# Optimization experiments

Measured on AMD Instinct MI355X. Metric: run time of the kernel, lower is better.

Reference implementation:

```python
import jax, jax.numpy as jnp
import numpy as np

# static multi-scale config (Deformable-DETR encoder, 1024x1024 image, strides 8/16/32/64)
SPATIAL_SHAPES = np.array([[128, 128], [64, 64], [32, 32], [16, 16]])  # (L, 2) = (h, w)
NUM_HEADS, NUM_LEVELS, NUM_POINTS = 8, 4, 4
EMBED, HEAD_DIM = 256, 32
NUM_KEYS = int(SPATIAL_SHAPES.prod(-1).sum())  # 21760


def _grid_sample(img, grid):
    """Bilinear grid_sample, padding_mode='zeros', align_corners=False.
    img: (BH, C, H, W); grid: (BH, Nq, P, 2) in [-1,1] -> (BH, C, Nq, P)."""
    BH, C, H, W = img.shape
    gx = (grid[..., 0] + 1.0) * (W / 2) - 0.5
    gy = (grid[..., 1] + 1.0) * (H / 2) - 0.5
    x0f, y0f = jnp.floor(gx), jnp.floor(gy)
    wx, wy = gx - x0f, gy - y0f
    x0, y0 = x0f.astype(jnp.int32), y0f.astype(jnp.int32)
    flat = img.reshape(BH, C, H * W)

    def gather(xi, yi, w):
        valid = (xi >= 0) & (xi < W) & (yi >= 0) & (yi < H)
        idx = jnp.clip(yi, 0, H - 1) * W + jnp.clip(xi, 0, W - 1)
        g = jnp.take_along_axis(flat, idx.reshape(BH, 1, -1), axis=2)
        g = g.reshape(BH, C, xi.shape[1], xi.shape[2])
        return g * (w * valid)[:, None]

    return (gather(x0, y0, (1 - wx) * (1 - wy)) + gather(x0 + 1, y0, wx * (1 - wy))
            + gather(x0, y0 + 1, (1 - wx) * wy) + gather(x0 + 1, y0 + 1, wx * wy))


def setup_inputs() -> dict:
    key = jax.random.key(0)
    ks = jax.random.split(key, 12)
    bs, nq = 1, NUM_KEYS
    s = 1.0 / np.sqrt(EMBED)
    return {
        "query": jax.random.normal(ks[0], (bs, nq, EMBED), jnp.float32),
        "query_pos": jax.random.normal(ks[1], (bs, nq, EMBED), jnp.float32),
        "value": jax.random.normal(ks[2], (bs, NUM_KEYS, EMBED), jnp.float32),
        "reference_points": jax.random.uniform(ks[3], (bs, nq, NUM_LEVELS, 2), jnp.float32),
        "spatial_shapes": jnp.asarray(SPATIAL_SHAPES, jnp.int32),
        "W_value": jax.random.normal(ks[4], (EMBED, EMBED), jnp.float32) * s,
        "b_value": jnp.zeros((EMBED,), jnp.float32),
        "W_off": jax.random.normal(ks[5], (NUM_HEADS * NUM_LEVELS * NUM_POINTS * 2, EMBED), jnp.float32) * 0.01,
        "b_off": jax.random.normal(ks[6], (NUM_HEADS * NUM_LEVELS * NUM_POINTS * 2,), jnp.float32),
        "W_attn": jax.random.normal(ks[7], (NUM_HEADS * NUM_LEVELS * NUM_POINTS, EMBED), jnp.float32) * s,
        "b_attn": jnp.zeros((NUM_HEADS * NUM_LEVELS * NUM_POINTS,), jnp.float32),
        "W_out": jax.random.normal(ks[8], (EMBED, EMBED), jnp.float32) * s,
        "b_out": jnp.zeros((EMBED,), jnp.float32),
    }


def reference(query, query_pos, value, reference_points, spatial_shapes,
              W_value, b_value, W_off, b_off, W_attn, b_attn, W_out, b_out):
    bs, nq, _ = query.shape
    identity = query
    q = query + query_pos  # pos_add
    v = value @ W_value.T + b_value  # value_proj: (bs, nk, E)
    v = v.reshape(bs, -1, NUM_HEADS, HEAD_DIM)

    offsets = (q @ W_off.T + b_off).reshape(bs, nq, NUM_HEADS, NUM_LEVELS, NUM_POINTS, 2)
    attn = (q @ W_attn.T + b_attn).reshape(bs, nq, NUM_HEADS, NUM_LEVELS * NUM_POINTS)
    attn = jax.nn.softmax(attn, axis=-1).reshape(bs, nq, NUM_HEADS, NUM_LEVELS, NUM_POINTS)

    # offset_normalizer = (w, h) per level; ref points are 2D -> loc = ref + off/norm
    normalizer = jnp.asarray(SPATIAL_SHAPES[:, ::-1].copy(), query.dtype)  # (L, 2)
    loc = reference_points[:, :, None, :, None, :] + offsets / normalizer[None, None, None, :, None, :]
    grids = 2.0 * loc - 1.0  # (bs, nq, H, L, P, 2)

    starts = np.concatenate([[0], np.cumsum(SPATIAL_SHAPES.prod(-1))])
    sampled = []
    for lvl in range(NUM_LEVELS):
        H_, W_ = int(SPATIAL_SHAPES[lvl, 0]), int(SPATIAL_SHAPES[lvl, 1])
        v_l = v[:, int(starts[lvl]):int(starts[lvl + 1])]  # (bs, H*W, heads, Dh)
        v_l = v_l.transpose(0, 2, 3, 1).reshape(bs * NUM_HEADS, HEAD_DIM, H_, W_)
        g_l = grids[:, :, :, lvl].transpose(0, 2, 1, 3, 4).reshape(bs * NUM_HEADS, nq, NUM_POINTS, 2)
        sampled.append(_grid_sample(v_l, g_l))  # (bs*H, Dh, nq, P)
    sampled = jnp.concatenate(sampled, axis=-1)  # (bs*H, Dh, nq, L*P)

    aw = attn.transpose(0, 2, 1, 3, 4).reshape(bs * NUM_HEADS, 1, nq, NUM_LEVELS * NUM_POINTS)
    out = (sampled * aw).sum(-1).reshape(bs, NUM_HEADS * HEAD_DIM, nq).transpose(0, 2, 1)
    out = out @ W_out.T + b_out  # output_proj
    return out + identity  # residual (dropout is identity at eval)
```

## Files before the change

kernel.cpp:

```cpp
#include <hip/hip_runtime.h>
#include <hip/hip_bf16.h>
#include <math.h>
#include <type_traits>

#define K_DIM 256
using bf16 = __hip_bfloat16;

typedef __attribute__((ext_vector_type(8))) short s8v;
typedef __attribute__((ext_vector_type(4))) float f4v;

__device__ __forceinline__ float b2f(unsigned short u) {
    return __uint_as_float(((unsigned)u) << 16);
}
__device__ __forceinline__ unsigned short f2b(float f) {
    unsigned u = __float_as_uint(f);
    unsigned r = 0x7FFFu + ((u >> 16) & 1u);
    return (unsigned short)((u + r) >> 16);
}
__device__ __forceinline__ float  ld1(const float* p) { return *p; }
__device__ __forceinline__ float  ld1(const bf16*  p) { return b2f(*(const unsigned short*)p); }
__device__ __forceinline__ float4 ld4(const float* p) { return *(const float4*)p; }
__device__ __forceinline__ float4 ld4(const bf16*  p) {
    ushort4 u = *(const ushort4*)p;
    return make_float4(b2f(u.x), b2f(u.y), b2f(u.z), b2f(u.w));
}
__device__ __forceinline__ s8v ldw8(const bf16* p) { return *(const s8v*)p; }

__device__ __forceinline__ bool detect_bf16(const unsigned* __restrict__ qw) {
    unsigned w = qw[threadIdx.x & 63];
    unsigned t = (w >> 8) & 0x7F;
    bool hit = (t >= 0x3Bu) && (t <= 0x42u);
    unsigned long long m = __ballot(hit);
    return __popcll(m) >= 32;
}

#define P1_TOTAL 164480
#define P_TOTAL  230272
__global__ __launch_bounds__(256) void k_prep(
    const unsigned* __restrict__ qd,
    const void* wv, const void* wo, const void* wa,
    const void* bv, const void* bo, const void* ba,
    const void* wout, const void* bout,
    bf16* __restrict__ dst1, bf16* __restrict__ dst2)
{
    const bool isb = detect_bf16(qd);
    const int i4 = (blockIdx.x * 256 + threadIdx.x) * 4;
    if (i4 >= P_TOTAL) return;
    const void* src; int off; bf16* dst;
    if (i4 < P1_TOTAL) {
        dst = dst1 + i4;
        if      (i4 < 65536)  { src = wv; off = i4; }
        else if (i4 < 131072) { src = wo; off = i4 - 65536; }
        else if (i4 < 163840) { src = wa; off = i4 - 131072; }
        else if (i4 < 164096) { src = bv; off = i4 - 163840; }
        else if (i4 < 164352) { src = bo; off = i4 - 164096; }
        else                  { src = ba; off = i4 - 164352; }
    } else {
        const int j = i4 - P1_TOTAL;
        dst = dst2 + j;
        if (j < 65536) { src = wout; off = j; }
        else           { src = bout; off = j - 65536; }
    }
    if (isb) {
        *(ushort4*)dst = *(const ushort4*)((const unsigned short*)src + off);
    } else {
        float4 v = *(const float4*)((const float*)src + off);
        *(ushort4*)dst = make_ushort4(f2b(v.x), f2b(v.y), f2b(v.z), f2b(v.w));
    }
}

template<typename AT, typename RT, typename CT, int NFRAG, bool ADD_A2, bool SPLIT,
         bool ADD_RES, bool HMAJOR, bool HM2, bool A1HM>
__device__ __forceinline__ void mfma_gemm_body(
    unsigned short* __restrict__ As, int bm,
    const AT* __restrict__ A1, const AT* __restrict__ A2,
    const bf16* __restrict__ W1, const bf16* __restrict__ bias1, CT* __restrict__ C1, int N1,
    const bf16* __restrict__ W2, const bf16* __restrict__ bias2, bf16* __restrict__ C2, int N2,
    const RT* __restrict__ Res, int Mtot)
{
    const int tid = threadIdx.x;

    {
        const AT* t1 = A1 + (size_t)bm * K_DIM;
        if constexpr (!ADD_A2 && std::is_same<AT, bf16>::value) {
            s8v r[4];
            #pragma unroll
            for (int j = 0; j < 4; ++j) {
                const int e = j * 2048 + tid * 8;
                const int row = e >> 8, col = e & 255;
                const bf16* src;
                if constexpr (A1HM)
                    src = (const bf16*)A1 +
                          ((size_t)(col >> 5) * (size_t)Mtot + (size_t)(bm + row)) * 32 + (col & 31);
                else
                    src = t1 + e;
                r[j] = *(const s8v*)src;
            }
            #pragma unroll
            for (int j = 0; j < 4; ++j) {
                const int e = j * 2048 + tid * 8;
                *(s8v*)&As[(e >> 8) * 264 + (e & 255)] = r[j];
            }
        } else {
            float4 ra[8], rb[8];
            #pragma unroll
            for (int j = 0; j < 8; ++j)
                ra[j] = ld4(t1 + j * 1024 + tid * 4);
            if (ADD_A2) {
                const AT* t2 = A2 + (size_t)bm * K_DIM;
                #pragma unroll
                for (int j = 0; j < 8; ++j)
                    rb[j] = ld4(t2 + j * 1024 + tid * 4);
            }
            #pragma unroll
            for (int j = 0; j < 8; ++j) {
                const int e = j * 1024 + tid * 4;
                float4 v = ra[j];
                if (ADD_A2) { v.x += rb[j].x; v.y += rb[j].y; v.z += rb[j].z; v.w += rb[j].w; }
                *(ushort4*)&As[(e >> 8) * 264 + (e & 255)] =
                    make_ushort4(f2b(v.x), f2b(v.y), f2b(v.z), f2b(v.w));
            }
        }
    }

    const int wv = tid >> 6;
    const int lane = tid & 63;
    const int n15 = lane & 15;
    const int quad = lane >> 4;

    const bf16* Wr[NFRAG];
    int col[NFRAG];
    #pragma unroll
    for (int f = 0; f < NFRAG; ++f) {
        const int c = (wv * NFRAG + f) * 16 + n15;
        col[f] = c;
        if (SPLIT && c >= N1) Wr[f] = W2 + (size_t)(c - N1) * K_DIM;
        else                  Wr[f] = W1 + (size_t)c * K_DIM;
    }

    s8v bcur[NFRAG], bnxt[NFRAG];
    #pragma unroll
    for (int f = 0; f < NFRAG; ++f) bcur[f] = ldw8(Wr[f] + quad * 8);

    float bv[NFRAG];
    #pragma unroll
    for (int f = 0; f < NFRAG; ++f) {
        const int c = col[f];
        const bool hi = SPLIT && (c >= N1);
        bv[f] = hi ? ld1(bias2 + (c - N1)) : ld1(bias1 + c);
    }

    float rres[NFRAG][8];
    if constexpr (ADD_RES) {
        #pragma unroll
        for (int f = 0; f < NFRAG; ++f)
            #pragma unroll
            for (int mi = 0; mi < 2; ++mi)
                #pragma unroll
                for (int r = 0; r < 4; ++r) {
                    const int m = bm + mi * 16 + quad * 4 + r;
                    rres[f][mi * 4 + r] = ld1(Res + (size_t)m * N1 + col[f]);
                }
    }

    __syncthreads();

    const f4v zz = {0.f, 0.f, 0.f, 0.f};
    f4v acc[2][NFRAG];
    #pragma unroll
    for (int mi = 0; mi < 2; ++mi)
        #pragma unroll
        for (int f = 0; f < NFRAG; ++f) acc[mi][f] = zz;

    #pragma unroll
    for (int kk = 0; kk < 8; ++kk) {
        const int k0 = kk * 32 + quad * 8;
        if (kk < 7) {
            #pragma unroll
            for (int f = 0; f < NFRAG; ++f) bnxt[f] = ldw8(Wr[f] + k0 + 32);
        }
        s8v a[2];
        #pragma unroll
        for (int mi = 0; mi < 2; ++mi)
            a[mi] = *(const s8v*)&As[(mi * 16 + n15) * 264 + k0];
        #pragma unroll
        for (int mi = 0; mi < 2; ++mi)
            #pragma unroll
            for (int f = 0; f < NFRAG; ++f)
                acc[mi][f] = __builtin_amdgcn_mfma_f32_16x16x32_bf16(a[mi], bcur[f], acc[mi][f], 0, 0, 0);
        if (kk < 7) {
            #pragma unroll
            for (int f = 0; f < NFRAG; ++f) bcur[f] = bnxt[f];
        }
    }

    __syncthreads();

    if constexpr (std::is_same<CT, float>::value) {
        float* Asf = (float*)As;
        #pragma unroll
        for (int pass = 0; pass < 2; ++pass) {
            #pragma unroll
            for (int f = 0; f < NFRAG; ++f)
                #pragma unroll
                for (int r = 0; r < 4; ++r) {
                    float v = acc[pass][f][r] + bv[f];
                    if (ADD_RES) v += rres[f][pass * 4 + r];
                    Asf[(quad * 4 + r) * 264 + col[f]] = v;
                }
            __syncthreads();
            {
                const int row = tid >> 4;
                const int c16 = tid & 15;
                float* dst = (float*)C1 + (size_t)(bm + pass * 16 + row) * 256;
                #pragma unroll
                for (int s = 0; s < 4; ++s) {
                    const int eo = (c16 + s * 16) * 4;
                    *(float4*)(dst + eo) = *(const float4*)(Asf + row * 264 + eo);
                }
            }
            __syncthreads();
        }
    } else {
        unsigned short* Asu = As;
        #pragma unroll
        for (int f = 0; f < NFRAG; ++f) {
            if (!SPLIT || col[f] < N1) {
                #pragma unroll
                for (int mi = 0; mi < 2; ++mi)
                    #pragma unroll
                    for (int r = 0; r < 4; ++r) {
                        float v = acc[mi][f][r] + bv[f];
                        if (ADD_RES) v += rres[f][mi * 4 + r];
                        Asu[(mi * 16 + quad * 4 + r) * 264 + col[f]] = f2b(v);
                    }
            }
        }
        __syncthreads();
        if constexpr (HMAJOR) {
            const int h = tid >> 5;
            const int t32 = tid & 31;
            bf16* dsth = C1 + ((size_t)h * Mtot + bm) * 32;
            #pragma unroll
            for (int s = 0; s < 4; ++s) {
                const int o16 = t32 + s * 32;
                const int row = o16 >> 2;
                const int ch8 = (o16 & 3) * 8;
                *(s8v*)(dsth + (size_t)row * 32 + ch8) =
                    *(const s8v*)(Asu + row * 264 + h * 32 + ch8);
            }
        } else {
            const int row = tid >> 3;
            const int c8 = tid & 7;
            bf16* dst = C1 + (size_t)(bm + row) * 256;
            #pragma unroll
            for (int s = 0; s < 4; ++s) {
                const int eo = (c8 + s * 8) * 8;
                *(s8v*)(dst + eo) = *(const s8v*)(Asu + row * 264 + eo);
            }
        }
        if constexpr (SPLIT) {
            __syncthreads();
            #pragma unroll
            for (int f = 0; f < NFRAG; ++f) {
                if (col[f] >= N1) {
                    #pragma unroll
                    for (int mi = 0; mi < 2; ++mi)
                        #pragma unroll
                        for (int r = 0; r < 4; ++r) {
                            float v = acc[mi][f][r] + bv[f];
                            Asu[(mi * 16 + quad * 4 + r) * 264 + (col[f] - N1)] = f2b(v);
                        }
                }
            }
            __syncthreads();
            const int h = tid >> 5;
            const int t32 = tid & 31;
            bf16* dsth = C2 + ((size_t)h * Mtot + bm) * 16;
            #pragma unroll
            for (int s = 0; s < 2; ++s) {
                const int o16 = t32 + s * 32;
                const int row = o16 >> 1;
                const int ch8 = (o16 & 1) * 8;
                *(s8v*)(dsth + (size_t)row * 16 + ch8) =
                    *(const s8v*)(Asu + row * 264 + h * 16 + ch8);
            }
        }
    }
}

__global__ __launch_bounds__(256) void k_gemm12(
    const unsigned* __restrict__ qd,
    const void* value, const void* query, const void* query_pos,
    const bf16* c_wv, const bf16* c_bv, bf16* vproj,
    const bf16* c_wo, const bf16* c_bo, bf16* osb,
    const bf16* c_wa, const bf16* c_ba, bf16* logit,
    int nb1, int Mtot)
{
    __shared__ __align__(16) unsigned short As[32 * 264];
    const bool isb = detect_bf16(qd);
    if ((int)blockIdx.x < nb1) {
        const int bm = blockIdx.x * 32;
        if (isb)
            mfma_gemm_body<bf16, float, bf16, 4, false, false, false, true, false, false>(As, bm,
                (const bf16*)value, nullptr, c_wv, c_bv, vproj, 256,
                nullptr, nullptr, nullptr, 0, nullptr, Mtot);
        else
            mfma_gemm_body<float, float, bf16, 4, false, false, false, true, false, false>(As, bm,
                (const float*)value, nullptr, c_wv, c_bv, vproj, 256,
                nullptr, nullptr, nullptr, 0, nullptr, Mtot);
    } else {
        const int bm = (blockIdx.x - nb1) * 32;
        if (isb)
            mfma_gemm_body<bf16, float, bf16, 6, true, true, false, true, true, false>(As, bm,
                (const bf16*)query, (const bf16*)query_pos, c_wo, c_bo, osb, 256,
                c_wa, c_ba, logit, 128, nullptr, Mtot);
        else
            mfma_gemm_body<float, float, bf16, 6, true, true, false, true, true, false>(As, bm,
                (const float*)query, (const float*)query_pos, c_wo, c_bo, osb, 256,
                c_wa, c_ba, logit, 128, nullptr, Mtot);
    }
}

__global__ __launch_bounds__(256) void k_gemm_final(
    const unsigned* __restrict__ qd, const bf16* A1,
    const bf16* W, const bf16* bias, const void* Res, void* C, int Mtot)
{
    __shared__ __align__(16) unsigned short As[32 * 264];
    const int bm = blockIdx.x * 32;
    if (detect_bf16(qd))
        mfma_gemm_body<bf16, bf16, bf16, 4, false, false, true, false, false, true>(As, bm,
            A1, nullptr, W, bias, (bf16*)C, 256,
            nullptr, nullptr, nullptr, 0, (const bf16*)Res, Mtot);
    else
        mfma_gemm_body<bf16, float, float, 4, false, false, true, false, false, true>(As, bm,
            A1, nullptr, W, bias, (float*)C, 256,
            nullptr, nullptr, nullptr, 0, (const float*)Res, Mtot);
}

struct SampLds {
    float    swgt[16][32][4];
    unsigned sidx[16][32][2];
};

__global__ __launch_bounds__(256) void k_sample(
    const unsigned* __restrict__ qd, const bf16* __restrict__ vproj,
    bf16* __restrict__ osb, const bf16* __restrict__ logits,
    const void* __restrict__ refp, int Mtot)
{
    __shared__ SampLds L;
    const bool isb = detect_bf16(qd);
    const int t  = threadIdx.x;
    const int p  = t >> 3;
    const int dg = t & 7;
    const int head = blockIdx.x & 7;
    const int qc   = blockIdx.x >> 3;
    const int q = qc * 32 + p;
    const size_t hm = (size_t)head * (size_t)Mtot;

    float f0, f1, f2, f3;
    {
        ushort4 u = *(const ushort4*)(osb + (hm + q) * 32 + dg * 4);
        f0 = b2f(u.x); f1 = b2f(u.y); f2 = b2f(u.z); f3 = b2f(u.w);
    }

    float p0, p1;
    {
        ushort2 lu = *(const ushort2*)(logits + (hm + q) * 16 + dg * 2);
        float l0 = b2f(lu.x), l1 = b2f(lu.y);
        float mx = fmaxf(l0, l1);
        mx = fmaxf(mx, __shfl_xor(mx, 1));
        mx = fmaxf(mx, __shfl_xor(mx, 2));
        mx = fmaxf(mx, __shfl_xor(mx, 4));
        float e0 = __expf(l0 - mx), e1 = __expf(l1 - mx);
        float s = e0 + e1;
        s += __shfl_xor(s, 1);
        s += __shfl_xor(s, 2);
        s += __shfl_xor(s, 4);
        const float inv = 1.f / s;
        p0 = e0 * inv; p1 = e1 * inv;
    }

    const int lv = dg >> 1;
    float rx, ry;
    if (isb) {
        rx = ld1((const bf16*)refp + (size_t)q * 8 + 2 * lv);
        ry = ld1((const bf16*)refp + (size_t)q * 8 + 2 * lv + 1);
    } else {
        rx = ld1((const float*)refp + (size_t)q * 8 + 2 * lv);
        ry = ld1((const float*)refp + (size_t)q * 8 + 2 * lv + 1);
    }

    #pragma unroll
    for (int tt = 0; tt < 2; ++tt) {
        const int i = dg * 2 + tt;
        const int l = i >> 2;
        const int WW = 128 >> l;
        const int st = (l == 0) ? 0 : (l == 1) ? 16384 : (l == 2) ? 20480 : 21504;
        const float ox = tt ? f2 : f0;
        const float oy = tt ? f3 : f1;
        const float aw = tt ? p1 : p0;
        const float gx = rx * (float)WW + ox - 0.5f;
        const float gy = ry * (float)WW + oy - 0.5f;
        const float x0f = floorf(gx);
        const float y0f = floorf(gy);
        const float wx = gx - x0f;
        const float wy = gy - y0f;
        const int x0 = (int)x0f;
        const int y0 = (int)y0f;
        const float ux0 = (x0 >= 0 && x0 < WW) ? (1.f - wx) : 0.f;
        const float ux1 = (x0 + 1 >= 0 && x0 + 1 < WW) ? wx : 0.f;
        const float uA = (x0 >= 0) ? ux0 : ux1;
        const float uB = (x0 >= 0) ? ux1 : 0.f;
        const int bx = min(max(x0, 0), WW - 1);
        const float vy0 = (y0 >= 0 && y0 < WW) ? 1.f : 0.f;
        const float vy1 = (y0 + 1 >= 0 && y0 + 1 < WW) ? 1.f : 0.f;
        const int yc0 = min(max(y0, 0), WW - 1);
        const int yc1 = min(max(y0 + 1, 0), WW - 1);
        const float cy0 = (1.f - wy) * vy0 * aw;
        const float cy1 = wy * vy1 * aw;
        *(float4*)L.swgt[i][p] = make_float4(uA * cy0, uB * cy0, uA * cy1, uB * cy1);
        *(uint2*)L.sidx[i][p] = make_uint2(
            (unsigned)(st + yc0 * WW + bx) * 64u,
            (unsigned)(st + yc1 * WW + bx) * 64u);
    }
    __syncthreads();

    const unsigned hb = (unsigned)(hm * 64) + (unsigned)dg * 16u;
    const char* vb = (const char*)vproj;

    uint2 iv[16];
    #pragma unroll
    for (int i = 0; i < 16; ++i) iv[i] = *(const uint2*)L.sidx[i][p];

    s8v r0[16], r1[16];
    #pragma unroll
    for (int i = 0; i < 16; ++i) {
        r0[i] = *(const s8v*)(vb + (size_t)(iv[i].x + hb));
        r1[i] = *(const s8v*)(vb + (size_t)(iv[i].y + hb));
    }

    const bool lo = (dg < 4);
    float acc[8] = {0.f, 0.f, 0.f, 0.f, 0.f, 0.f, 0.f, 0.f};
    #pragma unroll
    for (int i = 0; i < 16; ++i) {
        const float4 w = *(const float4*)L.swgt[i][p];
        const float w0 = lo ? w.x : w.y;
        const float w1 = lo ? w.z : w.w;
        #pragma unroll
        for (int k = 0; k < 8; ++k)
            acc[k] = fmaf(w0, b2f((unsigned short)r0[i][k]), acc[k]);
        #pragma unroll
        for (int k = 0; k < 8; ++k)
            acc[k] = fmaf(w1, b2f((unsigned short)r1[i][k]), acc[k]);
    }

    #pragma unroll
    for (int k = 0; k < 8; ++k) acc[k] += __shfl_xor(acc[k], 4);

    if (dg < 4) {
        s8v o;
        #pragma unroll
        for (int k = 0; k < 8; ++k) o[k] = (short)f2b(acc[k]);
        *(s8v*)(osb + (hm + q) * 32 + dg * 8) = o;
    }
}

extern "C" void kernel_launch(void* const* d_in, const int* in_sizes, int n_in,
                              void* d_out, int out_size, void* d_ws, size_t ws_size,
                              hipStream_t stream) {
    const void* query     = d_in[0];
    const void* query_pos = d_in[1];
    const void* value     = d_in[2];
    const void* refp      = d_in[3];
    const void* W_value = d_in[5];
    const void* b_value = d_in[6];
    const void* W_off   = d_in[7];
    const void* b_off   = d_in[8];
    const void* W_attn  = d_in[9];
    const void* b_attn  = d_in[10];
    const void* W_out   = d_in[11];
    const void* b_out   = d_in[12];
    const unsigned* qd = (const unsigned*)d_in[0];

    const int M = in_sizes[0] / 256;
    char* wsb = (char*)d_ws;

    bf16* vproj = (bf16*)wsb;
    bf16* osb   = (bf16*)(wsb + (size_t)M * 512);
    bf16* wc2   = (bf16*)(wsb + (size_t)M * 1024);
    bf16* logit = (bf16*)d_out;
    bf16* wc1   = (bf16*)((char*)d_out + (8u << 20));
    const bf16* c_wv = wc1;
    const bf16* c_wo = wc1 + 65536;
    const bf16* c_wa = wc1 + 131072;
    const bf16* c_bv = wc1 + 163840;
    const bf16* c_bo = wc1 + 164096;
    const bf16* c_ba = wc1 + 164352;

    dim3 blk(256, 1, 1);
    const int nb1 = M / 32;
    dim3 g12((unsigned)(2 * nb1), 1, 1);
    dim3 g32((unsigned)nb1, 1, 1);
    dim3 gs((unsigned)(M / 4), 1, 1);

    k_prep<<<dim3((P_TOTAL / 4 + 255) / 256), blk, 0, stream>>>(qd,
        W_value, W_off, W_attn, b_value, b_off, b_attn, W_out, b_out, wc1, wc2);
    k_gemm12<<<g12, blk, 0, stream>>>(qd, value, query, query_pos,
        c_wv, c_bv, vproj, c_wo, c_bo, osb, c_wa, c_ba, logit, nb1, M);
    k_sample<<<gs, blk, 0, stream>>>(qd, vproj, osb, logit, refp, M);
    k_gemm_final<<<g32, blk, 0, stream>>>(qd, osb, wc2, wc2 + 65536, query, d_out, M);
}
```

Baseline: 201.9 us.

## Double GEMM row tile to 64 and move residual add into coalesced epilogue

The GEMM body now processes 64 rows per block instead of 32, with four MFMA row fragments per wave, so each weight fragment loaded from global memory is reused across twice as many rows. This halves the block count and the total weight traffic. The residual is no longer gathered per element into registers before the main loop; it is read with vectorized, coalesced loads in a staged LDS epilogue and added there. The cost is more accumulator registers, a larger LDS tile and fewer blocks to spread across the GPU, which can lower occupancy.

```diff
diff --git a/kernel.cpp b/kernel.cpp
--- a/kernel.cpp
+++ b/kernel.cpp
@@ -83,9 +83,9 @@
     {
         const AT* t1 = A1 + (size_t)bm * K_DIM;
         if constexpr (!ADD_A2 && std::is_same<AT, bf16>::value) {
-            s8v r[4];
-            #pragma unroll
-            for (int j = 0; j < 4; ++j) {
+            s8v r[8];
+            #pragma unroll
+            for (int j = 0; j < 8; ++j) {
                 const int e = j * 2048 + tid * 8;
                 const int row = e >> 8, col = e & 255;
                 const bf16* src;
@@ -97,28 +97,31 @@
                 r[j] = *(const s8v*)src;
             }
             #pragma unroll
-            for (int j = 0; j < 4; ++j) {
+            for (int j = 0; j < 8; ++j) {
                 const int e = j * 2048 + tid * 8;
                 *(s8v*)&As[(e >> 8) * 264 + (e & 255)] = r[j];
             }
         } else {
-            float4 ra[8], rb[8];
-            #pragma unroll
-            for (int j = 0; j < 8; ++j)
-                ra[j] = ld4(t1 + j * 1024 + tid * 4);
-            if (ADD_A2) {
-                const AT* t2 = A2 + (size_t)bm * K_DIM;
+            const AT* t2 = ADD_A2 ? (A2 + (size_t)bm * K_DIM) : (const AT*)0;
+            #pragma unroll
+            for (int jb = 0; jb < 4; ++jb) {
+                float4 ra[4], rb[4];
                 #pragma unroll
-                for (int j = 0; j < 8; ++j)
-                    rb[j] = ld4(t2 + j * 1024 + tid * 4);
-            }
-            #pragma unroll
-            for (int j = 0; j < 8; ++j) {
-                const int e = j * 1024 + tid * 4;
-                float4 v = ra[j];
-                if (ADD_A2) { v.x += rb[j].x; v.y += rb[j].y; v.z += rb[j].z; v.w += rb[j].w; }
-                *(ushort4*)&As[(e >> 8) * 264 + (e & 255)] =
-                    make_ushort4(f2b(v.x), f2b(v.y), f2b(v.z), f2b(v.w));
+                for (int j = 0; j < 4; ++j)
+                    ra[j] = ld4(t1 + (jb * 4 + j) * 1024 + tid * 4);
+                if (ADD_A2) {
+                    #pragma unroll
+                    for (int j = 0; j < 4; ++j)
+                        rb[j] = ld4(t2 + (jb * 4 + j) * 1024 + tid * 4);
+                }
+                #pragma unroll
+                for (int j = 0; j < 4; ++j) {
+                    const int e = (jb * 4 + j) * 1024 + tid * 4;
+                    float4 v = ra[j];
+                    if (ADD_A2) { v.x += rb[j].x; v.y += rb[j].y; v.z += rb[j].z; v.w += rb[j].w; }
+                    *(ushort4*)&As[(e >> 8) * 264 + (e & 255)] =
+                        make_ushort4(f2b(v.x), f2b(v.y), f2b(v.z), f2b(v.w));
+                }
             }
         }
     }
@@ -150,25 +153,12 @@
         bv[f] = hi ? ld1(bias2 + (c - N1)) : ld1(bias1 + c);
     }
 
-    float rres[NFRAG][8];
-    if constexpr (ADD_RES) {
-        #pragma unroll
-        for (int f = 0; f < NFRAG; ++f)
-            #pragma unroll
-            for (int mi = 0; mi < 2; ++mi)
-                #pragma unroll
-                for (int r = 0; r < 4; ++r) {
-                    const int m = bm + mi * 16 + quad * 4 + r;
-                    rres[f][mi * 4 + r] = ld1(Res + (size_t)m * N1 + col[f]);
-                }
-    }
-
     __syncthreads();
 
     const f4v zz = {0.f, 0.f, 0.f, 0.f};
-    f4v acc[2][NFRAG];
-    #pragma unroll
-    for (int mi = 0; mi < 2; ++mi)
+    f4v acc[4][NFRAG];
+    #pragma unroll
+    for (int mi = 0; mi < 4; ++mi)
         #pragma unroll
         for (int f = 0; f < NFRAG; ++f) acc[mi][f] = zz;
 
@@ -179,12 +169,12 @@
             #pragma unroll
             for (int f = 0; f < NFRAG; ++f) bnxt[f] = ldw8(Wr[f] + k0 + 32);
         }
-        s8v a[2];
-        #pragma unroll
-        for (int mi = 0; mi < 2; ++mi)
+        s8v a[4];
+        #pragma unroll
+        for (int mi = 0; mi < 4; ++mi)
             a[mi] = *(const s8v*)&As[(mi * 16 + n15) * 264 + k0];
         #pragma unroll
-        for (int mi = 0; mi < 2; ++mi)
+        for (int mi = 0; mi < 4; ++mi)
             #pragma unroll
             for (int f = 0; f < NFRAG; ++f)
                 acc[mi][f] = __builtin_amdgcn_mfma_f32_16x16x32_bf16(a[mi], bcur[f], acc[mi][f], 0, 0, 0);
@@ -196,28 +186,35 @@
 
     __syncthreads();
 
-    if constexpr (std::is_same<CT, float>::value) {
+    if constexpr (ADD_RES) {
         float* Asf = (float*)As;
         #pragma unroll
-        for (int pass = 0; pass < 2; ++pass) {
+        for (int mi = 0; mi < 4; ++mi) {
             #pragma unroll
             for (int f = 0; f < NFRAG; ++f)
                 #pragma unroll
-                for (int r = 0; r < 4; ++r) {
-                    float v = acc[pass][f][r] + bv[f];
-                    if (ADD_RES) v += rres[f][pass * 4 + r];
-                    Asf[(quad * 4 + r) * 264 + col[f]] = v;
+                for (int r = 0; r < 4; ++r)
+                    Asf[(quad * 4 + r) * 264 + col[f]] = acc[mi][f][r] + bv[f];
+            __syncthreads();
+            #pragma unroll
+            for (int s = 0; s < 4; ++s) {
+                const int idx = s * 256 + tid;
+                const int row = idx >> 6;
+                const int c16 = idx & 63;
+                float4 o = *(const float4*)(Asf + row * 264 + c16 * 4);
+                const size_t m = (size_t)(bm + mi * 16 + row);
+                if constexpr (std::is_same<RT, bf16>::value) {
+                    ushort4 ru = *(const ushort4*)((const bf16*)Res + m * 256 + c16 * 4);
+                    o.x += b2f(ru.x); o.y += b2f(ru.y); o.z += b2f(ru.z); o.w += b2f(ru.w);
+                } else {
+                    float4 rf = *(const float4*)((const float*)Res + m * 256 + c16 * 4);
+                    o.x += rf.x; o.y += rf.y; o.z += rf.z; o.w += rf.w;
                 }
-            __syncthreads();
-            {
-                const int row = tid >> 4;
-                const int c16 = tid & 15;
-                float* dst = (float*)C1 + (size_t)(bm + pass * 16 + row) * 256;
-                #pragma unroll
-                for (int s = 0; s < 4; ++s) {
-                    const int eo = (c16 + s * 16) * 4;
-                    *(float4*)(dst + eo) = *(const float4*)(Asf + row * 264 + eo);
-                }
+                if constexpr (std::is_same<CT, float>::value)
+                    *(float4*)((float*)C1 + m * 256 + c16 * 4) = o;
+                else
+                    *(ushort4*)((bf16*)C1 + m * 256 + c16 * 4) =
+                        make_ushort4(f2b(o.x), f2b(o.y), f2b(o.z), f2b(o.w));
             }
             __syncthreads();
         }
@@ -227,13 +224,11 @@
         for (int f = 0; f < NFRAG; ++f) {
             if (!SPLIT || col[f] < N1) {
                 #pragma unroll
-                for (int mi = 0; mi < 2; ++mi)
+                for (int mi = 0; mi < 4; ++mi)
                     #pragma unroll
-                    for (int r = 0; r < 4; ++r) {
-                        float v = acc[mi][f][r] + bv[f];
-                        if (ADD_RES) v += rres[f][mi * 4 + r];
-                        Asu[(mi * 16 + quad * 4 + r) * 264 + col[f]] = f2b(v);
-                    }
+                    for (int r = 0; r < 4; ++r)
+                        Asu[(mi * 16 + quad * 4 + r) * 264 + col[f]] =
+                            f2b(acc[mi][f][r] + bv[f]);
             }
         }
         __syncthreads();
@@ -242,7 +237,7 @@
             const int t32 = tid & 31;
             bf16* dsth = C1 + ((size_t)h * Mtot + bm) * 32;
             #pragma unroll
-            for (int s = 0; s < 4; ++s) {
+            for (int s = 0; s < 8; ++s) {
                 const int o16 = t32 + s * 32;
                 const int row = o16 >> 2;
                 const int ch8 = (o16 & 3) * 8;
@@ -250,13 +245,13 @@
                     *(const s8v*)(Asu + row * 264 + h * 32 + ch8);
             }
         } else {
-            const int row = tid >> 3;
-            const int c8 = tid & 7;
-            bf16* dst = C1 + (size_t)(bm + row) * 256;
-            #pragma unroll
-            for (int s = 0; s < 4; ++s) {
-                const int eo = (c8 + s * 8) * 8;
-                *(s8v*)(dst + eo) = *(const s8v*)(Asu + row * 264 + eo);
+            #pragma unroll
+            for (int s = 0; s < 8; ++s) {
+                const int idx = s * 256 + tid;
+                const int row = idx >> 5;
+                const int c16 = idx & 31;
+                *(s8v*)(C1 + (size_t)(bm + row) * 256 + c16 * 8) =
+                    *(const s8v*)(Asu + row * 264 + c16 * 8);
             }
         }
         if constexpr (SPLIT) {
@@ -265,12 +260,11 @@
             for (int f = 0; f < NFRAG; ++f) {
                 if (col[f] >= N1) {
                     #pragma unroll
-                    for (int mi = 0; mi < 2; ++mi)
+                    for (int mi = 0; mi < 4; ++mi)
                         #pragma unroll
-                        for (int r = 0; r < 4; ++r) {
-                            float v = acc[mi][f][r] + bv[f];
-                            Asu[(mi * 16 + quad * 4 + r) * 264 + (col[f] - N1)] = f2b(v);
-                        }
+                        for (int r = 0; r < 4; ++r)
+                            Asu[(mi * 16 + quad * 4 + r) * 264 + (col[f] - N1)] =
+                                f2b(acc[mi][f][r] + bv[f]);
                 }
             }
             __syncthreads();
@@ -278,7 +272,7 @@
             const int t32 = tid & 31;
             bf16* dsth = C2 + ((size_t)h * Mtot + bm) * 16;
             #pragma unroll
-            for (int s = 0; s < 2; ++s) {
+            for (int s = 0; s < 4; ++s) {
                 const int o16 = t32 + s * 32;
                 const int row = o16 >> 1;
                 const int ch8 = (o16 & 1) * 8;
@@ -297,10 +291,10 @@
     const bf16* c_wa, const bf16* c_ba, bf16* logit,
     int nb1, int Mtot)
 {
-    __shared__ __align__(16) unsigned short As[32 * 264];
+    __shared__ __align__(16) unsigned short As[64 * 264];
     const bool isb = detect_bf16(qd);
     if ((int)blockIdx.x < nb1) {
-        const int bm = blockIdx.x * 32;
+        const int bm = blockIdx.x * 64;
         if (isb)
             mfma_gemm_body<bf16, float, bf16, 4, false, false, false, true, false, false>(As, bm,
                 (const bf16*)value, nullptr, c_wv, c_bv, vproj, 256,
@@ -310,7 +304,7 @@
                 (const float*)value, nullptr, c_wv, c_bv, vproj, 256,
                 nullptr, nullptr, nullptr, 0, nullptr, Mtot);
     } else {
-        const int bm = (blockIdx.x - nb1) * 32;
+        const int bm = (blockIdx.x - nb1) * 64;
         if (isb)
             mfma_gemm_body<bf16, float, bf16, 6, true, true, false, true, true, false>(As, bm,
                 (const bf16*)query, (const bf16*)query_pos, c_wo, c_bo, osb, 256,
@@ -326,8 +320,8 @@
     const unsigned* __restrict__ qd, const bf16* A1,
     const bf16* W, const bf16* bias, const void* Res, void* C, int Mtot)
 {
-    __shared__ __align__(16) unsigned short As[32 * 264];
-    const int bm = blockIdx.x * 32;
+    __shared__ __align__(16) unsigned short As[64 * 264];
+    const int bm = blockIdx.x * 64;
     if (detect_bf16(qd))
         mfma_gemm_body<bf16, bf16, bf16, 4, false, false, true, false, false, true>(As, bm,
             A1, nullptr, W, bias, (bf16*)C, 256,
@@ -499,9 +493,9 @@
     const bf16* c_ba = wc1 + 164352;
 
     dim3 blk(256, 1, 1);
-    const int nb1 = M / 32;
+    const int nb1 = M / 64;
     dim3 g12((unsigned)(2 * nb1), 1, 1);
-    dim3 g32((unsigned)nb1, 1, 1);
+    dim3 g64((unsigned)nb1, 1, 1);
     dim3 gs((unsigned)(M / 4), 1, 1);
 
     k_prep<<<dim3((P_TOTAL / 4 + 255) / 256), blk, 0, stream>>>(qd,
@@ -509,5 +503,5 @@
     k_gemm12<<<g12, blk, 0, stream>>>(qd, value, query, query_pos,
         c_wv, c_bv, vproj, c_wo, c_bo, osb, c_wa, c_ba, logit, nb1, M);
     k_sample<<<gs, blk, 0, stream>>>(qd, vproj, osb, logit, refp, M);
-    k_gemm_final<<<g32, blk, 0, stream>>>(qd, osb, wc2, wc2 + 65536, query, d_out, M);
-}
+    k_gemm_final<<<g64, blk, 0, stream>>>(qd, osb, wc2, wc2 + 65536, query, d_out, M);
+}
```

After: 194.5 us. 3.6% less time.
